# Kernel tuning notes

Hardware: AMD Instinct MI355X
Metric: run time of the kernel (lower is better)

Reference implementation:

```python
import jax, jax.numpy as jnp
import numpy as np

VOCAB = 50257
EMBED_DIM = 1024
FRONT_DIM = 2048  # int(embed_dim * front_embed_mul)
BATCH, SEQ = 4, 4096


def setup_inputs() -> dict:
    key = jax.random.key(0)
    k_idx, k_emb, k_w1, k_b1, k_w2, k_b2 = jax.random.split(key, 6)
    idxs = jax.random.randint(k_idx, (BATCH, SEQ), 0, VOCAB, dtype=jnp.int64)
    tok_embed = jax.random.normal(k_emb, (VOCAB, FRONT_DIM), dtype=jnp.float32)
    # torch nn.Linear weights are [out, in]
    W1 = jax.random.normal(k_w1, (EMBED_DIM, FRONT_DIM), dtype=jnp.float32) * (1.0 / np.sqrt(FRONT_DIM))
    b1 = jax.random.normal(k_b1, (EMBED_DIM,), dtype=jnp.float32) * 0.01
    W2 = jax.random.normal(k_w2, (EMBED_DIM, EMBED_DIM), dtype=jnp.float32) * (1.0 / np.sqrt(EMBED_DIM))
    b2 = jax.random.normal(k_b2, (EMBED_DIM,), dtype=jnp.float32) * 0.01
    return {"idxs": idxs, "tok_embed": tok_embed, "W1": W1, "b1": b1, "W2": W2, "b2": b2}


def reference(idxs, tok_embed, W1, b1, W2, b2):
    # Embedding gather: [B, S, front_dim]
    x = tok_embed[idxs]
    # integration1: Linear(front_dim -> embed_dim)
    x = jnp.einsum('bsf,ef->bse', x, W1) + b1
    # exact (erf-based) GELU, matching torch F.gelu default
    x = jax.nn.gelu(x, approximate=False)
    # integration2: Linear(embed_dim -> embed_dim)
    x = jnp.einsum('bse,oe->bso', x, W2) + b2
    return x
```

## Files before the change

kernel.cpp:

```cpp
#include <hip/hip_runtime.h>
#include <hip/hip_bf16.h>

typedef __attribute__((ext_vector_type(4))) float floatx4;
typedef __attribute__((ext_vector_type(8))) short short8;
typedef __attribute__((ext_vector_type(8))) unsigned short ushortx8;

#define K1 2048
#define N1 1024
#define K2 1024
#define N2 1024

__device__ __forceinline__ unsigned short f2bf(float f) {
  __hip_bfloat16 h = __float2bfloat16(f);
  return __builtin_bit_cast(unsigned short, h);
}

__device__ __forceinline__ void gload_lds16(const void* g, void* l) {
  __builtin_amdgcn_global_load_lds(
      (__attribute__((address_space(1))) void*)const_cast<void*>(g),
      (__attribute__((address_space(3))) void*)l, 16, 0, 0);
}

__global__ void cvt_bf16_kernel(const float* __restrict__ src,
                                unsigned short* __restrict__ dst, int n4) {
  int i = blockIdx.x * blockDim.x + threadIdx.x;
  if (i >= n4) return;
  float4 f = reinterpret_cast<const float4*>(src)[i];
  ushort4 o;
  o.x = f2bf(f.x); o.y = f2bf(f.y); o.z = f2bf(f.z); o.w = f2bf(f.w);
  reinterpret_cast<ushort4*>(dst)[i] = o;
}

__global__ __launch_bounds__(512, 2) void gemm1_fused_kernel(
    const int* __restrict__ idxs, const float* __restrict__ tok,
    const unsigned short* __restrict__ W1b, const float* __restrict__ b1,
    unsigned short* __restrict__ hout) {
  __shared__ unsigned short Asub[2][16384];
  __shared__ unsigned short Bsub[2][16384];
  const int t = threadIdx.x;
  const int p = blockIdx.x;
  const int bid = (p & 7) * 32 + (p >> 3);
  const int bm = bid >> 2, bn = bid & 3;
  const int brow0 = bm * 256, bcol0 = bn * 256;
  const int lane = t & 63, w = t >> 6;
  const int wm = w >> 2, wn = w & 3;
  const int fr = lane & 15, kg2 = lane >> 4;

  const int srow = t >> 3;
  const int cg = (t & 7) ^ (srow & 7);
  const float* aqf[4];
  const unsigned short* bq[4];
#pragma unroll
  for (int q = 0; q < 4; ++q) {
    const int ridx = idxs[brow0 + srow + 64 * q];
    aqf[q] = tok + (size_t)ridx * K1 + cg * 8;
    bq[q] = W1b + (size_t)(bcol0 + srow + 64 * q) * K1 + cg * 8;
  }
  const int t8 = t * 8;

  floatx4 acc[8][4] = {};
  constexpr int NT = K1 / 64;

  float4 av[4][2];
  auto loadA = [&](int k0) {
#pragma unroll
    for (int q = 0; q < 4; ++q) {
      av[q][0] = *reinterpret_cast<const float4*>(aqf[q] + k0);
      av[q][1] = *reinterpret_cast<const float4*>(aqf[q] + k0 + 4);
    }
  };
  auto writeA = [&](int d) {
#pragma unroll
    for (int q = 0; q < 4; ++q) {
      ushortx8 u;
      u[0] = f2bf(av[q][0].x); u[1] = f2bf(av[q][0].y);
      u[2] = f2bf(av[q][0].z); u[3] = f2bf(av[q][0].w);
      u[4] = f2bf(av[q][1].x); u[5] = f2bf(av[q][1].y);
      u[6] = f2bf(av[q][1].z); u[7] = f2bf(av[q][1].w);
      *reinterpret_cast<ushortx8*>(&Asub[d][t8 + q * 4096]) = u;
    }
  };
  auto issueB = [&](int d, int k0) {
#pragma unroll
    for (int q = 0; q < 4; ++q)
      gload_lds16(bq[q] + k0, &Bsub[d][t8 + q * 4096]);
  };
  auto computeKS = [&](int cur, int ks) {
    const int sl = ((ks * 4 + kg2) ^ (fr & 7)) * 8;
    short8 bf[4];
#pragma unroll
    for (int j = 0; j < 4; ++j)
      bf[j] = *(const short8*)&Bsub[cur][(wn * 64 + j * 16 + fr) * 64 + sl];
    __builtin_amdgcn_s_setprio(1);
#pragma unroll
    for (int i = 0; i < 8; ++i) {
      const short8 af = *(const short8*)&Asub[cur][(wm * 128 + i * 16 + fr) * 64 + sl];
#pragma unroll
      for (int j = 0; j < 4; ++j)
        acc[i][j] = __builtin_amdgcn_mfma_f32_16x16x32_bf16(af, bf[j], acc[i][j], 0, 0, 0);
    }
    __builtin_amdgcn_s_setprio(0);
  };

  loadA(0);
  issueB(0, 0);
  writeA(0);
  asm volatile("s_waitcnt vmcnt(0) lgkmcnt(0)\ns_barrier" ::: "memory");

#pragma unroll 1
  for (int tt = 0; tt < NT; ++tt) {
    const int cur = tt & 1;
    const int nbuf = cur ^ 1;
    const bool pf = (tt + 1 < NT);
    const int nk = (tt + 1) * 64;
    if (pf) {
      loadA(nk);
      issueB(nbuf, nk);
    }
    computeKS(cur, 0);
    if (pf) writeA(nbuf);
    computeKS(cur, 1);
    asm volatile("s_waitcnt vmcnt(0) lgkmcnt(0)\ns_barrier" ::: "memory");
  }

  const int er0 = brow0 + wm * 128 + kg2 * 4;
  const int ec0 = bcol0 + wn * 64 + fr;
#pragma unroll
  for (int j = 0; j < 4; ++j) {
    const float bv = b1[ec0 + j * 16];
#pragma unroll
    for (int i = 0; i < 8; ++i)
#pragma unroll
      for (int r = 0; r < 4; ++r) {
        float v = acc[i][j][r] + bv;
        v = 0.5f * v * (1.0f + erff(v * 0.70710678118654752f));
        hout[(size_t)(er0 + i * 16 + r) * N1 + (ec0 + j * 16)] = f2bf(v);
      }
  }
}

__global__ __launch_bounds__(512, 2) void gemm2_kernel(
    const unsigned short* __restrict__ A, const unsigned short* __restrict__ Bw,
    const float* __restrict__ bias, float* __restrict__ out) {
  __shared__ unsigned short Asub[2][16384];
  __shared__ unsigned short Bsub[2][16384];
  const int t = threadIdx.x;
  const int p = blockIdx.x;
  const int bid = (p & 7) * 32 + (p >> 3);
  const int bm = bid >> 2, bn = bid & 3;
  const int brow0 = bm * 256, bcol0 = bn * 256;
  const int lane = t & 63, w = t >> 6;
  const int wm = w >> 2, wn = w & 3;
  const int fr = lane & 15, kg2 = lane >> 4;

  const int srow = t >> 3;
  const int cg = (t & 7) ^ (srow & 7);
  const unsigned short* aq[4];
  const unsigned short* bq[4];
#pragma unroll
  for (int q = 0; q < 4; ++q) {
    aq[q] = A + (size_t)(brow0 + srow + 64 * q) * K2 + cg * 8;
    bq[q] = Bw + (size_t)(bcol0 + srow + 64 * q) * K2 + cg * 8;
  }
  const int t8 = t * 8;

  const int arow_sh = (wm * 128 + fr) * 64;
  const int brow_sh = (wn * 64 + fr) * 64;

  floatx4 acc[8][4] = {};
  constexpr int NT = K2 / 64;

  auto stage = [&](int d, int k0) {
#pragma unroll
    for (int q = 0; q < 4; ++q) {
      gload_lds16(aq[q] + k0, &Asub[d][t8 + q * 4096]);
      gload_lds16(bq[q] + k0, &Bsub[d][t8 + q * 4096]);
    }
  };
  auto compute = [&](int cur) {
#pragma unroll
    for (int ks = 0; ks < 2; ++ks) {
      const int sl = ((ks * 4 + kg2) ^ (fr & 7)) * 8;
      short8 bf[4];
#pragma unroll
      for (int j = 0; j < 4; ++j)
        bf[j] = *reinterpret_cast<const short8*>(&Bsub[cur][brow_sh + j * 1024 + sl]);
#pragma unroll
      for (int i = 0; i < 8; ++i) {
        const short8 af = *reinterpret_cast<const short8*>(&Asub[cur][arow_sh + i * 1024 + sl]);
#pragma unroll
        for (int j = 0; j < 4; ++j)
          acc[i][j] = __builtin_amdgcn_mfma_f32_16x16x32_bf16(af, bf[j], acc[i][j], 0, 0, 0);
      }
    }
  };

  stage(0, 0);
#pragma unroll 1
  for (int it = 0; it < NT - 1; ++it) {
    const int cur = it & 1;
    stage(cur ^ 1, (it + 1) * 64);
    asm volatile("s_waitcnt vmcnt(8)\ns_barrier" ::: "memory");
    compute(cur);
    asm volatile("s_waitcnt lgkmcnt(0)\ns_barrier" ::: "memory");
  }
  asm volatile("s_waitcnt vmcnt(0)\ns_barrier" ::: "memory");
  compute((NT - 1) & 1);

  const int er0 = brow0 + wm * 128 + kg2 * 4;
  const int ec0 = bcol0 + wn * 64 + fr;
#pragma unroll
  for (int j = 0; j < 4; ++j) {
    const float bv = bias[ec0 + j * 16];
#pragma unroll
    for (int i = 0; i < 8; ++i)
#pragma unroll
      for (int r = 0; r < 4; ++r)
        out[(size_t)(er0 + i * 16 + r) * N2 + (ec0 + j * 16)] = acc[i][j][r] + bv;
  }
}

extern "C" void kernel_launch(void* const* d_in, const int* in_sizes, int n_in,
                              void* d_out, int out_size, void* d_ws, size_t ws_size,
                              hipStream_t stream) {
  const int* idxs = (const int*)d_in[0];
  const float* tok = (const float*)d_in[1];
  const float* W1 = (const float*)d_in[2];
  const float* b1 = (const float*)d_in[3];
  const float* W2 = (const float*)d_in[4];
  const float* b2 = (const float*)d_in[5];
  float* out = (float*)d_out;

  unsigned short* W1b = (unsigned short*)d_ws;
  unsigned short* W2b = (unsigned short*)((char*)d_ws + (4u << 20));
  unsigned short* hbuf = (unsigned short*)((char*)d_ws + (6u << 20));

  cvt_bf16_kernel<<<2048, 256, 0, stream>>>(W1, W1b, 524288);
  cvt_bf16_kernel<<<1024, 256, 0, stream>>>(W2, W2b, 262144);
  gemm1_fused_kernel<<<256, 512, 0, stream>>>(idxs, tok, W1b, b1, hbuf);
  gemm2_kernel<<<256, 512, 0, stream>>>(hbuf, W2b, b2, out);
}
```

Baseline: 155.5 us.

## Deepen GEMM pipelines to 4-stage K=32 ring buffers with new LDS swizzles

Both GEMM kernels switch from a double-buffered K=64 tile to a 4-deep ring of K=32 tiles with three stages in flight, using vmcnt-based partial waits so global loads overlap more compute. GEMM1 also changes the gathered-embedding A path: each thread loads 16 floats of one row, A is stored in LDS with a padded 36-element row stride, and B uses a new XOR swizzle. The aim is to hide global-memory latency better, especially for the random-row embedding gather. The cost is one barrier per 32-wide K step instead of per 64, and more registers held for prefetched A data.

```diff
diff --git a/kernel.cpp b/kernel.cpp
--- a/kernel.cpp
+++ b/kernel.cpp
@@ -35,8 +35,8 @@
     const int* __restrict__ idxs, const float* __restrict__ tok,
     const unsigned short* __restrict__ W1b, const float* __restrict__ b1,
     unsigned short* __restrict__ hout) {
-  __shared__ unsigned short Asub[2][16384];
-  __shared__ unsigned short Bsub[2][16384];
+  __shared__ unsigned short As[4][9216];
+  __shared__ unsigned short Bs[4][8192];
   const int t = threadIdx.x;
   const int p = blockIdx.x;
   const int bid = (p & 7) * 32 + (p >> 3);
@@ -45,56 +45,54 @@
   const int lane = t & 63, w = t >> 6;
   const int wm = w >> 2, wn = w & 3;
   const int fr = lane & 15, kg2 = lane >> 4;
-
-  const int srow = t >> 3;
-  const int cg = (t & 7) ^ (srow & 7);
-  const float* aqf[4];
-  const unsigned short* bq[4];
-#pragma unroll
-  for (int q = 0; q < 4; ++q) {
-    const int ridx = idxs[brow0 + srow + 64 * q];
-    aqf[q] = tok + (size_t)ridx * K1 + cg * 8;
-    bq[q] = W1b + (size_t)(bcol0 + srow + 64 * q) * K1 + cg * 8;
-  }
+  const int slB = (kg2 ^ ((fr >> 1) & 3)) * 8;
+
+  const int ar = t >> 1;
+  const float* aptr = tok + (size_t)idxs[brow0 + ar] * K1 + (t & 1) * 16;
+  const int awr = ar * 36 + (t & 1) * 16;
+
+  const unsigned short* bptr[2];
+#pragma unroll
+  for (int j = 0; j < 2; ++j)
+    bptr[j] = W1b + (size_t)(bcol0 + j * 128 + (t >> 2)) * K1 +
+              ((t & 3) ^ ((t >> 3) & 3)) * 8;
   const int t8 = t * 8;
 
   floatx4 acc[8][4] = {};
-  constexpr int NT = K1 / 64;
-
-  float4 av[4][2];
-  auto loadA = [&](int k0) {
-#pragma unroll
-    for (int q = 0; q < 4; ++q) {
-      av[q][0] = *reinterpret_cast<const float4*>(aqf[q] + k0);
-      av[q][1] = *reinterpret_cast<const float4*>(aqf[q] + k0 + 4);
-    }
-  };
-  auto writeA = [&](int d) {
-#pragma unroll
-    for (int q = 0; q < 4; ++q) {
+  constexpr int NT = K1 / 32;
+
+  float4 av[2][4];
+  auto loadAv = [&](float4* dst, int k0) {
+#pragma unroll
+    for (int q = 0; q < 4; ++q)
+      dst[q] = *reinterpret_cast<const float4*>(aptr + k0 + q * 4);
+  };
+  auto writeAv = [&](int d, const float4* src) {
+#pragma unroll
+    for (int j = 0; j < 2; ++j) {
       ushortx8 u;
-      u[0] = f2bf(av[q][0].x); u[1] = f2bf(av[q][0].y);
-      u[2] = f2bf(av[q][0].z); u[3] = f2bf(av[q][0].w);
-      u[4] = f2bf(av[q][1].x); u[5] = f2bf(av[q][1].y);
-      u[6] = f2bf(av[q][1].z); u[7] = f2bf(av[q][1].w);
-      *reinterpret_cast<ushortx8*>(&Asub[d][t8 + q * 4096]) = u;
-    }
-  };
-  auto issueB = [&](int d, int k0) {
-#pragma unroll
-    for (int q = 0; q < 4; ++q)
-      gload_lds16(bq[q] + k0, &Bsub[d][t8 + q * 4096]);
-  };
-  auto computeKS = [&](int cur, int ks) {
-    const int sl = ((ks * 4 + kg2) ^ (fr & 7)) * 8;
+      u[0] = f2bf(src[2 * j].x); u[1] = f2bf(src[2 * j].y);
+      u[2] = f2bf(src[2 * j].z); u[3] = f2bf(src[2 * j].w);
+      u[4] = f2bf(src[2 * j + 1].x); u[5] = f2bf(src[2 * j + 1].y);
+      u[6] = f2bf(src[2 * j + 1].z); u[7] = f2bf(src[2 * j + 1].w);
+      *reinterpret_cast<ushortx8*>(&As[d][awr + j * 8]) = u;
+    }
+  };
+  auto gloadB = [&](int d, int k0) {
+#pragma unroll
+    for (int j = 0; j < 2; ++j)
+      gload_lds16(bptr[j] + k0, &Bs[d][j * 4096 + t8]);
+  };
+  auto compute = [&](int cur) {
     short8 bf[4];
 #pragma unroll
     for (int j = 0; j < 4; ++j)
-      bf[j] = *(const short8*)&Bsub[cur][(wn * 64 + j * 16 + fr) * 64 + sl];
+      bf[j] = *(const short8*)&Bs[cur][(wn * 64 + j * 16 + fr) * 32 + slB];
     __builtin_amdgcn_s_setprio(1);
 #pragma unroll
     for (int i = 0; i < 8; ++i) {
-      const short8 af = *(const short8*)&Asub[cur][(wm * 128 + i * 16 + fr) * 64 + sl];
+      const short8 af =
+          *(const short8*)&As[cur][(wm * 128 + i * 16 + fr) * 36 + kg2 * 8];
 #pragma unroll
       for (int j = 0; j < 4; ++j)
         acc[i][j] = __builtin_amdgcn_mfma_f32_16x16x32_bf16(af, bf[j], acc[i][j], 0, 0, 0);
@@ -102,25 +100,30 @@
     __builtin_amdgcn_s_setprio(0);
   };
 
-  loadA(0);
-  issueB(0, 0);
-  writeA(0);
-  asm volatile("s_waitcnt vmcnt(0) lgkmcnt(0)\ns_barrier" ::: "memory");
-
-#pragma unroll 1
+  {
+    float4 tv[4];
+    loadAv(tv, 0);
+    gloadB(0, 0); gloadB(1, 32); gloadB(2, 64);
+    loadAv(av[0], 32);
+    loadAv(av[1], 64);
+    writeAv(0, tv);
+    asm volatile("s_waitcnt vmcnt(0) lgkmcnt(0)\ns_barrier" ::: "memory");
+  }
+
+#pragma unroll 2
   for (int tt = 0; tt < NT; ++tt) {
-    const int cur = tt & 1;
-    const int nbuf = cur ^ 1;
-    const bool pf = (tt + 1 < NT);
-    const int nk = (tt + 1) * 64;
-    if (pf) {
-      loadA(nk);
-      issueB(nbuf, nk);
-    }
-    computeKS(cur, 0);
-    if (pf) writeA(nbuf);
-    computeKS(cur, 1);
-    asm volatile("s_waitcnt vmcnt(0) lgkmcnt(0)\ns_barrier" ::: "memory");
+    if (tt < NT - 2)
+      asm volatile("s_waitcnt vmcnt(12) lgkmcnt(0)\ns_barrier" ::: "memory");
+    else if (tt == NT - 2)
+      asm volatile("s_waitcnt vmcnt(6) lgkmcnt(0)\ns_barrier" ::: "memory");
+    else
+      asm volatile("s_waitcnt vmcnt(0) lgkmcnt(0)\ns_barrier" ::: "memory");
+    if (tt + 1 < NT) writeAv((tt + 1) & 3, av[tt & 1]);
+    if (tt + 3 < NT) {
+      loadAv(av[tt & 1], (tt + 3) * 32);
+      gloadB((tt + 3) & 3, (tt + 3) * 32);
+    }
+    compute(tt & 3);
   }
 
   const int er0 = brow0 + wm * 128 + kg2 * 4;
@@ -140,10 +143,10 @@
 }
 
 __global__ __launch_bounds__(512, 2) void gemm2_kernel(
-    const unsigned short* __restrict__ A, const unsigned short* __restrict__ Bw,
-    const float* __restrict__ bias, float* __restrict__ out) {
-  __shared__ unsigned short Asub[2][16384];
-  __shared__ unsigned short Bsub[2][16384];
+    const unsigned short* __restrict__ hb, const unsigned short* __restrict__ W2b,
+    const float* __restrict__ b2, float* __restrict__ out) {
+  __shared__ unsigned short As[4][8192];
+  __shared__ unsigned short Bs[4][8192];
   const int t = threadIdx.x;
   const int p = blockIdx.x;
   const int bid = (p & 7) * 32 + (p >> 3);
@@ -152,66 +155,66 @@
   const int lane = t & 63, w = t >> 6;
   const int wm = w >> 2, wn = w & 3;
   const int fr = lane & 15, kg2 = lane >> 4;
-
-  const int srow = t >> 3;
-  const int cg = (t & 7) ^ (srow & 7);
-  const unsigned short* aq[4];
-  const unsigned short* bq[4];
-#pragma unroll
-  for (int q = 0; q < 4; ++q) {
-    aq[q] = A + (size_t)(brow0 + srow + 64 * q) * K2 + cg * 8;
-    bq[q] = Bw + (size_t)(bcol0 + srow + 64 * q) * K2 + cg * 8;
+  const int slB = (kg2 ^ ((fr >> 1) & 3)) * 8;
+
+  const unsigned short* aptr[2];
+  const unsigned short* bptr[2];
+#pragma unroll
+  for (int j = 0; j < 2; ++j) {
+    const int row = j * 128 + (t >> 2);
+    const int cS = ((t & 3) ^ ((t >> 3) & 3)) * 8;
+    aptr[j] = hb + (size_t)(brow0 + row) * K2 + cS;
+    bptr[j] = W2b + (size_t)(bcol0 + row) * K2 + cS;
   }
   const int t8 = t * 8;
 
-  const int arow_sh = (wm * 128 + fr) * 64;
-  const int brow_sh = (wn * 64 + fr) * 64;
-
   floatx4 acc[8][4] = {};
-  constexpr int NT = K2 / 64;
+  constexpr int NT = K2 / 32;
 
   auto stage = [&](int d, int k0) {
 #pragma unroll
-    for (int q = 0; q < 4; ++q) {
-      gload_lds16(aq[q] + k0, &Asub[d][t8 + q * 4096]);
-      gload_lds16(bq[q] + k0, &Bsub[d][t8 + q * 4096]);
+    for (int j = 0; j < 2; ++j) {
+      gload_lds16(aptr[j] + k0, &As[d][j * 4096 + t8]);
+      gload_lds16(bptr[j] + k0, &Bs[d][j * 4096 + t8]);
     }
   };
   auto compute = [&](int cur) {
-#pragma unroll
-    for (int ks = 0; ks < 2; ++ks) {
-      const int sl = ((ks * 4 + kg2) ^ (fr & 7)) * 8;
-      short8 bf[4];
+    short8 bf[4];
+#pragma unroll
+    for (int j = 0; j < 4; ++j)
+      bf[j] = *(const short8*)&Bs[cur][(wn * 64 + j * 16 + fr) * 32 + slB];
+    __builtin_amdgcn_s_setprio(1);
+#pragma unroll
+    for (int i = 0; i < 8; ++i) {
+      const short8 af =
+          *(const short8*)&As[cur][(wm * 128 + i * 16 + fr) * 32 + slB];
 #pragma unroll
       for (int j = 0; j < 4; ++j)
-        bf[j] = *reinterpret_cast<const short8*>(&Bsub[cur][brow_sh + j * 1024 + sl]);
-#pragma unroll
-      for (int i = 0; i < 8; ++i) {
-        const short8 af = *reinterpret_cast<const short8*>(&Asub[cur][arow_sh + i * 1024 + sl]);
-#pragma unroll
-        for (int j = 0; j < 4; ++j)
-          acc[i][j] = __builtin_amdgcn_mfma_f32_16x16x32_bf16(af, bf[j], acc[i][j], 0, 0, 0);
-      }
-    }
-  };
-
-  stage(0, 0);
+        acc[i][j] = __builtin_amdgcn_mfma_f32_16x16x32_bf16(af, bf[j], acc[i][j], 0, 0, 0);
+    }
+    __builtin_amdgcn_s_setprio(0);
+  };
+
+  stage(0, 0); stage(1, 32); stage(2, 64);
+  asm volatile("s_waitcnt vmcnt(0) lgkmcnt(0)\ns_barrier" ::: "memory");
+
 #pragma unroll 1
-  for (int it = 0; it < NT - 1; ++it) {
-    const int cur = it & 1;
-    stage(cur ^ 1, (it + 1) * 64);
-    asm volatile("s_waitcnt vmcnt(8)\ns_barrier" ::: "memory");
-    compute(cur);
-    asm volatile("s_waitcnt lgkmcnt(0)\ns_barrier" ::: "memory");
-  }
-  asm volatile("s_waitcnt vmcnt(0)\ns_barrier" ::: "memory");
-  compute((NT - 1) & 1);
+  for (int tt = 0; tt < NT; ++tt) {
+    if (tt < NT - 2)
+      asm volatile("s_waitcnt vmcnt(8) lgkmcnt(0)\ns_barrier" ::: "memory");
+    else if (tt == NT - 2)
+      asm volatile("s_waitcnt vmcnt(4) lgkmcnt(0)\ns_barrier" ::: "memory");
+    else
+      asm volatile("s_waitcnt vmcnt(0) lgkmcnt(0)\ns_barrier" ::: "memory");
+    if (tt + 3 < NT) stage((tt + 3) & 3, (tt + 3) * 32);
+    compute(tt & 3);
+  }
 
   const int er0 = brow0 + wm * 128 + kg2 * 4;
   const int ec0 = bcol0 + wn * 64 + fr;
 #pragma unroll
   for (int j = 0; j < 4; ++j) {
-    const float bv = bias[ec0 + j * 16];
+    const float bv = b2[ec0 + j * 16];
 #pragma unroll
     for (int i = 0; i < 8; ++i)
 #pragma unroll
```

Result: slower. 197.1 us (+26.7%).

## Split next-stage prefetch to issue one chunk before the wait barrier

Applied to the files above, without the earlier changes.

Both GEMM main loops are restructured so each iteration starts with an LDS-drain barrier. The first chunk of the next stage's global-to-LDS loads is issued next, then a partial vmcnt wait and a second barrier confirm the current buffer is ready, and only then are the remaining chunks issued. The aim is to start next-stage memory traffic earlier and overlap it with the wait on the current stage. It also adds MFMA priority raising in the second GEMM. The cost is an extra barrier per iteration in each loop, and the schedule relies on exact vmcnt counts.

```diff
diff --git a/kernel.cpp b/kernel.cpp
--- a/kernel.cpp
+++ b/kernel.cpp
@@ -80,10 +80,13 @@
       *reinterpret_cast<ushortx8*>(&Asub[d][t8 + q * 4096]) = u;
     }
   };
-  auto issueB = [&](int d, int k0) {
-#pragma unroll
-    for (int q = 0; q < 4; ++q)
-      gload_lds16(bq[q] + k0, &Bsub[d][t8 + q * 4096]);
+  auto issueBq = [&](int d, int k0, int q) {
+    switch (q) {
+      case 0: gload_lds16(bq[0] + k0, &Bsub[d][t8]); break;
+      case 1: gload_lds16(bq[1] + k0, &Bsub[d][t8 + 4096]); break;
+      case 2: gload_lds16(bq[2] + k0, &Bsub[d][t8 + 8192]); break;
+      default: gload_lds16(bq[3] + k0, &Bsub[d][t8 + 12288]); break;
+    }
   };
   auto computeKS = [&](int cur, int ks) {
     const int sl = ((ks * 4 + kg2) ^ (fr & 7)) * 8;
@@ -103,9 +106,8 @@
   };
 
   loadA(0);
-  issueB(0, 0);
+  issueBq(0, 0, 0); issueBq(0, 0, 1); issueBq(0, 0, 2); issueBq(0, 0, 3);
   writeA(0);
-  asm volatile("s_waitcnt vmcnt(0) lgkmcnt(0)\ns_barrier" ::: "memory");
 
 #pragma unroll 1
   for (int tt = 0; tt < NT; ++tt) {
@@ -113,14 +115,20 @@
     const int nbuf = cur ^ 1;
     const bool pf = (tt + 1 < NT);
     const int nk = (tt + 1) * 64;
+    asm volatile("s_waitcnt lgkmcnt(0)\ns_barrier" ::: "memory");
+    if (pf) {
+      issueBq(nbuf, nk, 0);
+      asm volatile("s_waitcnt vmcnt(1)\ns_barrier" ::: "memory");
+    } else {
+      asm volatile("s_waitcnt vmcnt(0)\ns_barrier" ::: "memory");
+    }
     if (pf) {
       loadA(nk);
-      issueB(nbuf, nk);
+      issueBq(nbuf, nk, 1); issueBq(nbuf, nk, 2); issueBq(nbuf, nk, 3);
     }
     computeKS(cur, 0);
     if (pf) writeA(nbuf);
     computeKS(cur, 1);
-    asm volatile("s_waitcnt vmcnt(0) lgkmcnt(0)\ns_barrier" ::: "memory");
   }
 
   const int er0 = brow0 + wm * 128 + kg2 * 4;
@@ -170,9 +178,13 @@
   floatx4 acc[8][4] = {};
   constexpr int NT = K2 / 64;
 
-  auto stage = [&](int d, int k0) {
-#pragma unroll
-    for (int q = 0; q < 4; ++q) {
+  auto stage0 = [&](int d, int k0) {
+    gload_lds16(aq[0] + k0, &Asub[d][t8]);
+    gload_lds16(bq[0] + k0, &Bsub[d][t8]);
+  };
+  auto stageRest = [&](int d, int k0) {
+#pragma unroll
+    for (int q = 1; q < 4; ++q) {
       gload_lds16(aq[q] + k0, &Asub[d][t8 + q * 4096]);
       gload_lds16(bq[q] + k0, &Bsub[d][t8 + q * 4096]);
     }
@@ -185,6 +197,7 @@
 #pragma unroll
       for (int j = 0; j < 4; ++j)
         bf[j] = *reinterpret_cast<const short8*>(&Bsub[cur][brow_sh + j * 1024 + sl]);
+      __builtin_amdgcn_s_setprio(1);
 #pragma unroll
       for (int i = 0; i < 8; ++i) {
         const short8 af = *reinterpret_cast<const short8*>(&Asub[cur][arow_sh + i * 1024 + sl]);
@@ -192,20 +205,29 @@
         for (int j = 0; j < 4; ++j)
           acc[i][j] = __builtin_amdgcn_mfma_f32_16x16x32_bf16(af, bf[j], acc[i][j], 0, 0, 0);
       }
-    }
-  };
-
-  stage(0, 0);
+      __builtin_amdgcn_s_setprio(0);
+    }
+  };
+
+  stage0(0, 0);
+  stageRest(0, 0);
+
 #pragma unroll 1
-  for (int it = 0; it < NT - 1; ++it) {
-    const int cur = it & 1;
-    stage(cur ^ 1, (it + 1) * 64);
-    asm volatile("s_waitcnt vmcnt(8)\ns_barrier" ::: "memory");
+  for (int tt = 0; tt < NT; ++tt) {
+    const int cur = tt & 1;
+    const int nbuf = cur ^ 1;
+    const bool pf = (tt + 1 < NT);
+    const int nk = (tt + 1) * 64;
+    asm volatile("s_waitcnt lgkmcnt(0)\ns_barrier" ::: "memory");
+    if (pf) {
+      stage0(nbuf, nk);
+      asm volatile("s_waitcnt vmcnt(2)\ns_barrier" ::: "memory");
+    } else {
+      asm volatile("s_waitcnt vmcnt(0)\ns_barrier" ::: "memory");
+    }
+    if (pf) stageRest(nbuf, nk);
     compute(cur);
-    asm volatile("s_waitcnt lgkmcnt(0)\ns_barrier" ::: "memory");
-  }
-  asm volatile("s_waitcnt vmcnt(0)\ns_barrier" ::: "memory");
-  compute((NT - 1) & 1);
+  }
 
   const int er0 = brow0 + wm * 128 + kg2 * 4;
   const int ec0 = bcol0 + wn * 64 + fr;
```

New measurement: 161.1 us. 3.6% more time.

## Reshape GEMM block tiles to 128x512 with one wave per column strip

Applied to the files above, without the earlier changes.

Both GEMMs change from 256x256 block tiles, where waves form a 2x4 grid, to 128x512 tiles, where each of the 8 waves owns a 64-column strip across all 128 rows. Each block now converts only 128 gathered fp32 embedding rows per k-step instead of 256, so per-thread gather and conversion work drops and the full weight tile is read into LDS through direct global-to-LDS loads. The cost is more weight traffic per block, since B is 512 rows deep, and the tile is more rectangular. gemm2 also gets s_setprio around its MFMA loop and a wait count adjusted for the new load count.

```diff
diff --git a/kernel.cpp b/kernel.cpp
--- a/kernel.cpp
+++ b/kernel.cpp
@@ -1,5 +1,6 @@
 #include <hip/hip_runtime.h>
 #include <hip/hip_bf16.h>
+
 
 typedef __attribute__((ext_vector_type(4))) float floatx4;
 typedef __attribute__((ext_vector_type(8))) short short8;
@@ -35,66 +36,63 @@
     const int* __restrict__ idxs, const float* __restrict__ tok,
     const unsigned short* __restrict__ W1b, const float* __restrict__ b1,
     unsigned short* __restrict__ hout) {
-  __shared__ unsigned short Asub[2][16384];
-  __shared__ unsigned short Bsub[2][16384];
+  __shared__ unsigned short As[2][8192];
+  __shared__ unsigned short Bs[2][32768];
   const int t = threadIdx.x;
   const int p = blockIdx.x;
   const int bid = (p & 7) * 32 + (p >> 3);
-  const int bm = bid >> 2, bn = bid & 3;
-  const int brow0 = bm * 256, bcol0 = bn * 256;
+  const int bm = bid >> 1, bn = bid & 1;
+  const int brow0 = bm * 128, bcol0 = bn * 512;
   const int lane = t & 63, w = t >> 6;
-  const int wm = w >> 2, wn = w & 3;
+  const int wn = w;
   const int fr = lane & 15, kg2 = lane >> 4;
 
   const int srow = t >> 3;
   const int cg = (t & 7) ^ (srow & 7);
-  const float* aqf[4];
-  const unsigned short* bq[4];
-#pragma unroll
-  for (int q = 0; q < 4; ++q) {
-    const int ridx = idxs[brow0 + srow + 64 * q];
-    aqf[q] = tok + (size_t)ridx * K1 + cg * 8;
-    bq[q] = W1b + (size_t)(bcol0 + srow + 64 * q) * K1 + cg * 8;
-  }
+  const float* aqf[2];
+  aqf[0] = tok + (size_t)idxs[brow0 + srow] * K1 + cg * 8;
+  aqf[1] = tok + (size_t)idxs[brow0 + 64 + srow] * K1 + cg * 8;
+  const unsigned short* bq = W1b + (size_t)(bcol0 + srow) * K1 + cg * 8;
   const int t8 = t * 8;
 
   floatx4 acc[8][4] = {};
   constexpr int NT = K1 / 64;
 
-  float4 av[4][2];
+  float4 av[2][2];
   auto loadA = [&](int k0) {
 #pragma unroll
-    for (int q = 0; q < 4; ++q) {
-      av[q][0] = *reinterpret_cast<const float4*>(aqf[q] + k0);
-      av[q][1] = *reinterpret_cast<const float4*>(aqf[q] + k0 + 4);
+    for (int s = 0; s < 2; ++s) {
+      av[s][0] = *reinterpret_cast<const float4*>(aqf[s] + k0);
+      av[s][1] = *reinterpret_cast<const float4*>(aqf[s] + k0 + 4);
     }
   };
   auto writeA = [&](int d) {
 #pragma unroll
-    for (int q = 0; q < 4; ++q) {
+    for (int s = 0; s < 2; ++s) {
       ushortx8 u;
-      u[0] = f2bf(av[q][0].x); u[1] = f2bf(av[q][0].y);
-      u[2] = f2bf(av[q][0].z); u[3] = f2bf(av[q][0].w);
-      u[4] = f2bf(av[q][1].x); u[5] = f2bf(av[q][1].y);
-      u[6] = f2bf(av[q][1].z); u[7] = f2bf(av[q][1].w);
-      *reinterpret_cast<ushortx8*>(&Asub[d][t8 + q * 4096]) = u;
+      u[0] = f2bf(av[s][0].x); u[1] = f2bf(av[s][0].y);
+      u[2] = f2bf(av[s][0].z); u[3] = f2bf(av[s][0].w);
+      u[4] = f2bf(av[s][1].x); u[5] = f2bf(av[s][1].y);
+      u[6] = f2bf(av[s][1].z); u[7] = f2bf(av[s][1].w);
+      *reinterpret_cast<ushortx8*>(&As[d][s * 4096 + t8]) = u;
     }
   };
   auto issueB = [&](int d, int k0) {
 #pragma unroll
-    for (int q = 0; q < 4; ++q)
-      gload_lds16(bq[q] + k0, &Bsub[d][t8 + q * 4096]);
+    for (int q = 0; q < 8; ++q)
+      gload_lds16(bq + (size_t)q * 64 * K1 + k0, &Bs[d][q * 4096 + t8]);
   };
   auto computeKS = [&](int cur, int ks) {
     const int sl = ((ks * 4 + kg2) ^ (fr & 7)) * 8;
     short8 bf[4];
 #pragma unroll
     for (int j = 0; j < 4; ++j)
-      bf[j] = *(const short8*)&Bsub[cur][(wn * 64 + j * 16 + fr) * 64 + sl];
+      bf[j] = *(const short8*)&Bs[cur][wn * 4096 + (j * 16 + fr) * 64 + sl];
     __builtin_amdgcn_s_setprio(1);
 #pragma unroll
     for (int i = 0; i < 8; ++i) {
-      const short8 af = *(const short8*)&Asub[cur][(wm * 128 + i * 16 + fr) * 64 + sl];
+      const short8 af = *(const short8*)
+          &As[cur][(i >> 2) * 4096 + ((i & 3) * 16 + fr) * 64 + sl];
 #pragma unroll
       for (int j = 0; j < 4; ++j)
         acc[i][j] = __builtin_amdgcn_mfma_f32_16x16x32_bf16(af, bf[j], acc[i][j], 0, 0, 0);
@@ -123,7 +121,7 @@
     asm volatile("s_waitcnt vmcnt(0) lgkmcnt(0)\ns_barrier" ::: "memory");
   }
 
-  const int er0 = brow0 + wm * 128 + kg2 * 4;
+  const int er0 = brow0 + kg2 * 4;
   const int ec0 = bcol0 + wn * 64 + fr;
 #pragma unroll
   for (int j = 0; j < 4; ++j) {
@@ -140,42 +138,37 @@
 }
 
 __global__ __launch_bounds__(512, 2) void gemm2_kernel(
-    const unsigned short* __restrict__ A, const unsigned short* __restrict__ Bw,
-    const float* __restrict__ bias, float* __restrict__ out) {
-  __shared__ unsigned short Asub[2][16384];
-  __shared__ unsigned short Bsub[2][16384];
+    const unsigned short* __restrict__ hb, const unsigned short* __restrict__ W2b,
+    const float* __restrict__ b2, float* __restrict__ out) {
+  __shared__ unsigned short As[2][8192];
+  __shared__ unsigned short Bs[2][32768];
   const int t = threadIdx.x;
   const int p = blockIdx.x;
   const int bid = (p & 7) * 32 + (p >> 3);
-  const int bm = bid >> 2, bn = bid & 3;
-  const int brow0 = bm * 256, bcol0 = bn * 256;
+  const int bm = bid >> 1, bn = bid & 1;
+  const int brow0 = bm * 128, bcol0 = bn * 512;
   const int lane = t & 63, w = t >> 6;
-  const int wm = w >> 2, wn = w & 3;
+  const int wn = w;
   const int fr = lane & 15, kg2 = lane >> 4;
 
   const int srow = t >> 3;
   const int cg = (t & 7) ^ (srow & 7);
-  const unsigned short* aq[4];
-  const unsigned short* bq[4];
-#pragma unroll
-  for (int q = 0; q < 4; ++q) {
-    aq[q] = A + (size_t)(brow0 + srow + 64 * q) * K2 + cg * 8;
-    bq[q] = Bw + (size_t)(bcol0 + srow + 64 * q) * K2 + cg * 8;
-  }
+  const unsigned short* aq[2];
+  aq[0] = hb + (size_t)(brow0 + srow) * K2 + cg * 8;
+  aq[1] = hb + (size_t)(brow0 + 64 + srow) * K2 + cg * 8;
+  const unsigned short* bq = W2b + (size_t)(bcol0 + srow) * K2 + cg * 8;
   const int t8 = t * 8;
-
-  const int arow_sh = (wm * 128 + fr) * 64;
-  const int brow_sh = (wn * 64 + fr) * 64;
 
   floatx4 acc[8][4] = {};
   constexpr int NT = K2 / 64;
 
   auto stage = [&](int d, int k0) {
 #pragma unroll
-    for (int q = 0; q < 4; ++q) {
-      gload_lds16(aq[q] + k0, &Asub[d][t8 + q * 4096]);
-      gload_lds16(bq[q] + k0, &Bsub[d][t8 + q * 4096]);
-    }
+    for (int s = 0; s < 2; ++s)
+      gload_lds16(aq[s] + k0, &As[d][s * 4096 + t8]);
+#pragma unroll
+    for (int q = 0; q < 8; ++q)
+      gload_lds16(bq + (size_t)q * 64 * K2 + k0, &Bs[d][q * 4096 + t8]);
   };
   auto compute = [&](int cur) {
 #pragma unroll
@@ -184,14 +177,17 @@
       short8 bf[4];
 #pragma unroll
       for (int j = 0; j < 4; ++j)
-        bf[j] = *reinterpret_cast<const short8*>(&Bsub[cur][brow_sh + j * 1024 + sl]);
+        bf[j] = *(const short8*)&Bs[cur][wn * 4096 + (j * 16 + fr) * 64 + sl];
+      __builtin_amdgcn_s_setprio(1);
 #pragma unroll
       for (int i = 0; i < 8; ++i) {
-        const short8 af = *reinterpret_cast<const short8*>(&Asub[cur][arow_sh + i * 1024 + sl]);
+        const short8 af = *(const short8*)
+            &As[cur][(i >> 2) * 4096 + ((i & 3) * 16 + fr) * 64 + sl];
 #pragma unroll
         for (int j = 0; j < 4; ++j)
           acc[i][j] = __builtin_amdgcn_mfma_f32_16x16x32_bf16(af, bf[j], acc[i][j], 0, 0, 0);
       }
+      __builtin_amdgcn_s_setprio(0);
     }
   };
 
@@ -200,18 +196,18 @@
   for (int it = 0; it < NT - 1; ++it) {
     const int cur = it & 1;
     stage(cur ^ 1, (it + 1) * 64);
-    asm volatile("s_waitcnt vmcnt(8)\ns_barrier" ::: "memory");
+    asm volatile("s_waitcnt vmcnt(10)\ns_barrier" ::: "memory");
     compute(cur);
     asm volatile("s_waitcnt lgkmcnt(0)\ns_barrier" ::: "memory");
   }
   asm volatile("s_waitcnt vmcnt(0)\ns_barrier" ::: "memory");
   compute((NT - 1) & 1);
 
-  const int er0 = brow0 + wm * 128 + kg2 * 4;
+  const int er0 = brow0 + kg2 * 4;
   const int ec0 = bcol0 + wn * 64 + fr;
 #pragma unroll
   for (int j = 0; j < 4; ++j) {
-    const float bv = bias[ec0 + j * 16];
+    const float bv = b2[ec0 + j * 16];
 #pragma unroll
     for (int i = 0; i < 8; ++i)
 #pragma unroll
```

After: 157.4 us. About the same (+1.2%).
